# Kernel optimization log

Hardware: AMD Instinct MI355X
Metric: run time of the kernel (lower is better)

Reference implementation:

```python
import jax, jax.numpy as jnp
import numpy as np

B, N, M, C = 8, 2048, 2048, 512


def setup_inputs() -> dict:
    key = jax.random.key(0)
    ks = jax.random.split(key, 10)
    s = 1.0 / np.sqrt(C)
    dec_embed = jax.random.normal(ks[0], (B, N, C), dtype=jnp.float32)
    enc_embed = jax.random.normal(ks[1], (B, M, C), dtype=jnp.float32)
    trans_mat = (jax.random.uniform(ks[2], (B, N, M)) < 0.5).astype(jnp.float32)
    Wv = jax.random.uniform(ks[3], (C, C), minval=-s, maxval=s, dtype=jnp.float32)
    bv = jax.random.uniform(ks[4], (C,), minval=-s, maxval=s, dtype=jnp.float32)
    W1 = jax.random.uniform(ks[5], (C, C), minval=-s, maxval=s, dtype=jnp.float32)
    b1 = jax.random.uniform(ks[6], (C,), minval=-s, maxval=s, dtype=jnp.float32)
    W2 = jax.random.uniform(ks[7], (C, C), minval=-s, maxval=s, dtype=jnp.float32)
    b2 = jax.random.uniform(ks[8], (C,), minval=-s, maxval=s, dtype=jnp.float32)
    return {"dec_embed": dec_embed, "enc_embed": enc_embed, "trans_mat": trans_mat,
            "Wv": Wv, "bv": bv, "W1": W1, "b1": b1, "W2": W2, "b2": b2}


def reference(dec_embed, enc_embed, trans_mat, Wv, bv, W1, b1, W2, b2):
    # scores [B,N,M], elementwise-masked by trans_mat
    attn = jnp.einsum('bnc,bmc->bnm', dec_embed, enc_embed) * trans_mat
    # NONSTANDARD masked softmax: zeros participate in softmax (exp(0)=1 in denom),
    # then positions where attn==0 are re-zeroed.
    sm = jax.nn.softmax(attn, axis=-1)
    attn = jnp.where(attn != 0, sm, jnp.zeros((), attn.dtype))
    v = enc_embed @ Wv + bv                      # [B,M,C]
    v = jnp.tanh(jnp.einsum('bnm,bmc->bnc', attn, v))  # [B,N,C]
    g = dec_embed * v + dec_embed                # tanh-gate + residual
    h = jax.nn.relu(g @ W1 + b1)                 # Mlp fc1 + ReLU (drop=0)
    return h @ W2 + b2                           # Mlp fc2
```

## Files before the change

### kernel.cpp

```cpp
#include <hip/hip_runtime.h>
#include <math.h>

#define Bb 8
#define Nn 2048
#define Mm 2048
#define Cc 512

typedef __attribute__((ext_vector_type(8))) _Float16 hfrag;
typedef __attribute__((ext_vector_type(4))) float f4;
typedef __attribute__((ext_vector_type(4))) _Float16 h4;

__device__ __forceinline__ void gld16(const void* g, void* l) {
    __builtin_amdgcn_global_load_lds(
        (const __attribute__((address_space(1))) void*)g,
        (__attribute__((address_space(3))) void*)l, 16, 0, 0);
}

template<int EPI, int BN, int SWZ>
__global__ __launch_bounds__(256) void gemm_mfma(
    const _Float16* __restrict__ Ah, long sA, int lda,
    const _Float16* __restrict__ Bh, long sB, int ldb,
    const float* __restrict__ aux, long sAux, int ldaux,
    const _Float16* __restrict__ aux2,
    float* __restrict__ mlal,
    void* __restrict__ Cout, long sC, int ldc, int K, int GX)
{
    constexpr int NI = (BN == 128) ? 4 : 2;
    constexpr int NQ = (512 + BN * 4) / 256;

    __shared__ _Float16 As[128 * 32];
    __shared__ _Float16 Bs[BN * 32];

    int bx, by, bz;
    if (SWZ == 1) {
        const int id = blockIdx.x;
        bz = id & 7; bx = (id >> 3) % GX; by = (id >> 3) / GX;
    } else if (SWZ == 2) {
        const int id = blockIdx.x;
        bz = 0; bx = (id >> 3) % GX; by = (id & 7) + 8 * ((id >> 3) / GX);
    } else {
        bx = blockIdx.x; by = blockIdx.y; bz = 0;
    }

    const _Float16* A0 = Ah + (size_t)bz * sA;
    const _Float16* B0 = Bh + (size_t)bz * sB;

    const int tid  = threadIdx.x;
    const int wv   = tid >> 6;
    const int ln   = tid & 63;
    const int wx   = (BN == 128) ? (wv & 1) : 0;
    const int wy   = (BN == 128) ? (wv >> 1) : wv;
    const int lcol = ln & 15, quad = ln >> 4;
    const int row0w = wy * (NI * 16);
    const int col0w = wx * 64;

    const int rowBase = by * 128;
    const int colBase = bx * BN;

    f4 acc[NI][4];
    const f4 z4 = {0.f, 0.f, 0.f, 0.f};
    #pragma unroll
    for (int i = 0; i < NI; ++i)
        #pragma unroll
        for (int j = 0; j < 4; ++j) acc[i][j] = z4;

    const float* alb = (EPI == 2) ? (mlal + (size_t)bz * (2048 * 32)) : nullptr;
    _Float16 als[4] = {(_Float16)0.f, (_Float16)0.f, (_Float16)0.f, (_Float16)0.f};

    for (int k0 = 0; k0 < K; k0 += 32) {
        __syncthreads();
        #pragma unroll
        for (int q = 0; q < NQ; ++q) {
            const int c0 = q * 256 + wv * 64;
            const int c  = c0 + ln;
            if (c0 < 512) {
                const int r  = c >> 2;
                const int ko = (c & 3) * 8;
                gld16(A0 + (size_t)(rowBase + r) * lda + k0 + ko, &As[c0 * 8]);
            } else {
                const int cb = c - 512;
                const int r  = cb >> 2;
                const int ko = (cb & 3) * 8;
                gld16(B0 + (size_t)(colBase + r) * ldb + k0 + ko, &Bs[(c0 - 512) * 8]);
            }
        }
        __syncthreads();

        hfrag af[NI], bf_[4];
        const int aoff = quad * 8;
        #pragma unroll
        for (int i = 0; i < NI; ++i)
            af[i]  = *(const hfrag*)&As[(row0w + i * 16 + lcol) * 32 + aoff];
        #pragma unroll
        for (int j = 0; j < 4; ++j)
            bf_[j] = *(const hfrag*)&Bs[(col0w + j * 16 + lcol) * 32 + aoff];

        if (EPI == 2) {
            if ((k0 & 63) == 0) {
                const int t = k0 >> 6;
                #pragma unroll
                for (int j = 0; j < 4; ++j) {
                    const int n = colBase + col0w + j * 16 + lcol;
                    als[j] = (_Float16)alb[(size_t)n * 32 + t];
                }
            }
            #pragma unroll
            for (int j = 0; j < 4; ++j) bf_[j] = bf_[j] * als[j];
        }

        #pragma unroll
        for (int i = 0; i < NI; ++i)
            #pragma unroll
            for (int j = 0; j < 4; ++j)
                acc[i][j] = __builtin_amdgcn_mfma_f32_16x16x32_f16(af[i], bf_[j], acc[i][j], 0, 0, 0);
    }

    const int crow0 = rowBase + row0w + quad * 4;
    const int ccol0 = colBase + col0w + lcol;

    if (EPI == 0) {
        _Float16* E = (_Float16*)Cout + (size_t)bz * sC;
        const float* Mk = aux + (size_t)bz * sAux;
        #pragma unroll
        for (int i = 0; i < NI; ++i) {
            const int m0r = crow0 + i * 16;
            #pragma unroll
            for (int j = 0; j < 4; ++j) {
                const int n = ccol0 + j * 16;
                const f4 mk = *(const f4*)(Mk + (size_t)n * ldaux + m0r);
                #pragma unroll
                for (int r = 0; r < 4; ++r) acc[i][j][r] *= mk[r];
            }
        }
        const int t = (rowBase + row0w) >> 6;
        #pragma unroll
        for (int j = 0; j < 4; ++j) {
            const int n = ccol0 + j * 16;
            float mx = acc[0][j][0];
            #pragma unroll
            for (int i = 0; i < NI; ++i)
                #pragma unroll
                for (int r = 0; r < 4; ++r) mx = fmaxf(mx, acc[i][j][r]);
            mx = fmaxf(mx, __shfl_xor(mx, 16, 64));
            mx = fmaxf(mx, __shfl_xor(mx, 32, 64));
            float l0 = 0.f;
            #pragma unroll
            for (int i = 0; i < NI; ++i) {
                h4 ev;
                #pragma unroll
                for (int r = 0; r < 4; ++r) {
                    const float s = acc[i][j][r];
                    const float e = __expf(s - mx);
                    l0 += e;
                    ev[r] = (s == 0.f) ? (_Float16)0.f : (_Float16)e;
                }
                *(h4*)(E + (size_t)n * ldc + crow0 + i * 16) = ev;
            }
            l0 += __shfl_xor(l0, 16, 64);
            l0 += __shfl_xor(l0, 32, 64);
            if (quad == 0) {
                float2 p; p.x = mx; p.y = l0;
                ((float2*)mlal)[((size_t)bz * 2048 + n) * 32 + t] = p;
            }
        }
    } else if (EPI == 1) {
        _Float16* C = (_Float16*)Cout;
        #pragma unroll
        for (int j = 0; j < 4; ++j) {
            const int col = ccol0 + j * 16;
            const float bi = aux[col];
            #pragma unroll
            for (int i = 0; i < NI; ++i) {
                const int rowb = crow0 + i * 16;
                const int bb = rowb >> 11, ml = rowb & 2047;
                h4 st;
                #pragma unroll
                for (int r = 0; r < 4; ++r) st[r] = (_Float16)(acc[i][j][r] + bi);
                *(h4*)(C + (size_t)bb * ((size_t)Cc * Mm) + (size_t)col * Mm + ml) = st;
            }
        }
    } else if (EPI == 2) {
        _Float16* C = (_Float16*)Cout + (size_t)bz * sC;
        const _Float16* Dg = aux2 + (size_t)bz * sC;
        #pragma unroll
        for (int i = 0; i < NI; ++i) {
            const int c0 = crow0 + i * 16;
            #pragma unroll
            for (int j = 0; j < 4; ++j) {
                const int n = ccol0 + j * 16;
                const h4 dv = *(const h4*)(Dg + (size_t)n * ldc + c0);
                h4 gv;
                #pragma unroll
                for (int r = 0; r < 4; ++r) {
                    const float a = acc[i][j][r];
                    const float th = 1.f - 2.f / (__expf(2.f * a) + 1.f);
                    gv[r] = (_Float16)((float)dv[r] * (1.f + th));
                }
                *(h4*)(C + (size_t)n * ldc + c0) = gv;
            }
        }
    } else if (EPI == 3) {
        _Float16* C = (_Float16*)Cout;
        #pragma unroll
        for (int i = 0; i < NI; ++i) {
            const int c0 = crow0 + i * 16;
            const f4 bi = *(const f4*)(aux + c0);
            #pragma unroll
            for (int j = 0; j < 4; ++j) {
                const int n = ccol0 + j * 16;
                h4 hv;
                #pragma unroll
                for (int r = 0; r < 4; ++r)
                    hv[r] = (_Float16)fmaxf(acc[i][j][r] + bi[r], 0.f);
                *(h4*)(C + (size_t)n * ldc + c0) = hv;
            }
        }
    } else {
        float* C = (float*)Cout;
        #pragma unroll
        for (int i = 0; i < NI; ++i) {
            const int c0 = crow0 + i * 16;
            const f4 bi = *(const f4*)(aux + c0);
            #pragma unroll
            for (int j = 0; j < 4; ++j) {
                const int n = ccol0 + j * 16;
                f4 ov;
                #pragma unroll
                for (int r = 0; r < 4; ++r) ov[r] = acc[i][j][r] + bi[r];
                *(f4*)(C + (size_t)n * ldc + c0) = ov;
            }
        }
    }
}

__global__ __launch_bounds__(64) void combine_kernel(
    const float* __restrict__ mlq, float* __restrict__ alpha)
{
    const int row = blockIdx.x * 64 + threadIdx.x;
    const float2* ml = (const float2*)mlq + (size_t)row * 32;
    float mt[32], lt[32];
    float m = -1e30f;
    #pragma unroll
    for (int t = 0; t < 32; ++t) {
        float2 p = ml[t];
        mt[t] = p.x; lt[t] = p.y;
        m = fmaxf(m, p.x);
    }
    float et[32], l = 0.f;
    #pragma unroll
    for (int t = 0; t < 32; ++t) {
        et[t] = __expf(mt[t] - m);
        l += lt[t] * et[t];
    }
    const float inv = 1.f / l;
    float* ap = alpha + (size_t)row * 32;
    #pragma unroll
    for (int t = 0; t < 32; ++t) ap[t] = et[t] * inv;
}

__global__ __launch_bounds__(256) void sconv(const float* __restrict__ x,
                                             _Float16* __restrict__ o)
{
    const size_t i = (size_t)blockIdx.x * 256 + threadIdx.x;
    f4 v = ((const f4*)x)[i];
    h4 hh;
    #pragma unroll
    for (int k = 0; k < 4; ++k) hh[k] = (_Float16)v[k];
    ((h4*)o)[i] = hh;
}

__global__ __launch_bounds__(256) void wconv(const float* s0, const float* s1, const float* s2,
                                             _Float16* d0, _Float16* d1, _Float16* d2)
{
    const float* Sm = blockIdx.z == 0 ? s0 : blockIdx.z == 1 ? s1 : s2;
    _Float16* D = blockIdx.z == 0 ? d0 : blockIdx.z == 1 ? d1 : d2;
    __shared__ float t[32][33];
    const int x = threadIdx.x & 31, y = threadIdx.x >> 5;
    const int gx = blockIdx.x * 32, gy = blockIdx.y * 32;
    #pragma unroll
    for (int yy = y; yy < 32; yy += 8)
        t[yy][x] = Sm[(size_t)(gy + yy) * 512 + gx + x];
    __syncthreads();
    #pragma unroll
    for (int yy = y; yy < 32; yy += 8)
        D[(size_t)(gx + yy) * 512 + gy + x] = (_Float16)t[x][yy];
}

extern "C" void kernel_launch(void* const* d_in, const int* in_sizes, int n_in,
                              void* d_out, int out_size, void* d_ws, size_t ws_size,
                              hipStream_t stream)
{
    const float* dec   = (const float*)d_in[0];
    const float* enc   = (const float*)d_in[1];
    const float* trans = (const float*)d_in[2];
    const float* Wv = (const float*)d_in[3];
    const float* bv = (const float*)d_in[4];
    const float* W1 = (const float*)d_in[5];
    const float* b1 = (const float*)d_in[6];
    const float* W2 = (const float*)d_in[7];
    const float* b2 = (const float*)d_in[8];

    char* ws = (char*)d_ws;
    _Float16* e     = (_Float16*)ws;
    float*    mlq   = (float*)(ws + 0x4000000);
    float*    alpha = (float*)(ws + 0x4400000);
    _Float16* dec_h = (_Float16*)(ws + 0x4600000);
    _Float16* Wvt   = (_Float16*)(ws + 0x5600000);
    _Float16* W1t   = Wvt + 262144;
    _Float16* W2t   = Wvt + 524288;
    _Float16* vT    = (_Float16*)(ws + 0x5800000);
    _Float16* g     = (_Float16*)(ws + 0x6800000);
    _Float16* h     = (_Float16*)(ws + 0x7800000);
    _Float16* enc_h = (_Float16*)d_out;

    sconv<<<dim3(8192), 256, 0, stream>>>(dec, dec_h);
    sconv<<<dim3(8192), 256, 0, stream>>>(enc, enc_h);
    wconv<<<dim3(16, 16, 3), 256, 0, stream>>>(Wv, W1, W2, Wvt, W1t, W2t);

    gemm_mfma<0, 128, 1><<<dim3(2048), 256, 0, stream>>>(
        enc_h, (long)Mm * Cc, 512,
        dec_h, (long)Nn * Cc, 512,
        trans, (long)Nn * Mm, 2048, nullptr, mlq,
        e, (long)Nn * Mm, 2048, 512, 16);

    combine_kernel<<<dim3(256), 64, 0, stream>>>(mlq, alpha);

    gemm_mfma<1, 64, 2><<<dim3(1024), 256, 0, stream>>>(
        enc_h, 0, 512, Wvt, 0, 512, bv, 0, 0, nullptr, nullptr,
        vT, 0, 0, 512, 8);

    gemm_mfma<2, 128, 1><<<dim3(512), 256, 0, stream>>>(
        vT, (long)Cc * Mm, 2048,
        e, (long)Nn * Mm, 2048,
        nullptr, 0, 512, dec_h, alpha,
        g, (long)Nn * Cc, 512, 2048, 16);

    gemm_mfma<3, 64, 0><<<dim3(256, 4), 256, 0, stream>>>(
        W1t, 0, 512, g, 0, 512, b1, 0, 0, nullptr, nullptr,
        h, 0, 512, 512, 0);

    gemm_mfma<4, 64, 0><<<dim3(256, 4), 256, 0, stream>>>(
        W2t, 0, 512, h, 0, 512, b2, 0, 0, nullptr, nullptr,
        d_out, 0, 512, 512, 0);
}
```

Baseline: 460.3 us.

## Double K-tile depth per sync and software-pipeline mask loads in softmax epilogue

The GEMM main loop now stages a 64-wide K slice (two 32-wide halves) into doubled LDS buffers per iteration, which halves the number of barrier pairs and global-to-LDS issue rounds. The EPI==2 alpha scale load is hoisted to once per 64-K step. In the EPI==0 epilogue, mask loads are restructured so the loads for the next column group are issued before the current group's max/exp work, letting their latency overlap. The cost is more LDS per block and more registers live in the epilogue, which may reduce occupancy.

After: 436.4 us. 5.2% less time.

```diff
diff --git a/kernel.cpp b/kernel.cpp
--- a/kernel.cpp
+++ b/kernel.cpp
@@ -26,10 +26,10 @@
     void* __restrict__ Cout, long sC, int ldc, int K, int GX)
 {
     constexpr int NI = (BN == 128) ? 4 : 2;
-    constexpr int NQ = (512 + BN * 4) / 256;
-
-    __shared__ _Float16 As[128 * 32];
-    __shared__ _Float16 Bs[BN * 32];
+    constexpr int NQ = (1024 + BN * 8) / 256;
+
+    __shared__ _Float16 As[2 * 128 * 32];
+    __shared__ _Float16 Bs[2 * BN * 32];
 
     int bx, by, bz;
     if (SWZ == 1) {
@@ -67,52 +67,58 @@
     const float* alb = (EPI == 2) ? (mlal + (size_t)bz * (2048 * 32)) : nullptr;
     _Float16 als[4] = {(_Float16)0.f, (_Float16)0.f, (_Float16)0.f, (_Float16)0.f};
 
-    for (int k0 = 0; k0 < K; k0 += 32) {
+    for (int k0 = 0; k0 < K; k0 += 64) {
         __syncthreads();
         #pragma unroll
         for (int q = 0; q < NQ; ++q) {
             const int c0 = q * 256 + wv * 64;
             const int c  = c0 + ln;
-            if (c0 < 512) {
-                const int r  = c >> 2;
-                const int ko = (c & 3) * 8;
+            if (c0 < 1024) {
+                const int hh = c >> 9;
+                const int r  = (c >> 2) & 127;
+                const int ko = hh * 32 + (c & 3) * 8;
                 gld16(A0 + (size_t)(rowBase + r) * lda + k0 + ko, &As[c0 * 8]);
             } else {
-                const int cb = c - 512;
-                const int r  = cb >> 2;
-                const int ko = (cb & 3) * 8;
-                gld16(B0 + (size_t)(colBase + r) * ldb + k0 + ko, &Bs[(c0 - 512) * 8]);
+                const int cb = c - 1024;
+                const int hh = cb / (BN * 4);
+                const int r  = (cb >> 2) & (BN - 1);
+                const int ko = hh * 32 + (cb & 3) * 8;
+                gld16(B0 + (size_t)(colBase + r) * ldb + k0 + ko, &Bs[(c0 - 1024) * 8]);
             }
         }
         __syncthreads();
 
-        hfrag af[NI], bf_[4];
-        const int aoff = quad * 8;
-        #pragma unroll
-        for (int i = 0; i < NI; ++i)
-            af[i]  = *(const hfrag*)&As[(row0w + i * 16 + lcol) * 32 + aoff];
-        #pragma unroll
-        for (int j = 0; j < 4; ++j)
-            bf_[j] = *(const hfrag*)&Bs[(col0w + j * 16 + lcol) * 32 + aoff];
-
         if (EPI == 2) {
-            if ((k0 & 63) == 0) {
-                const int t = k0 >> 6;
-                #pragma unroll
-                for (int j = 0; j < 4; ++j) {
-                    const int n = colBase + col0w + j * 16 + lcol;
-                    als[j] = (_Float16)alb[(size_t)n * 32 + t];
-                }
-            }
-            #pragma unroll
-            for (int j = 0; j < 4; ++j) bf_[j] = bf_[j] * als[j];
-        }
-
-        #pragma unroll
-        for (int i = 0; i < NI; ++i)
+            const int t = k0 >> 6;
+            #pragma unroll
+            for (int j = 0; j < 4; ++j) {
+                const int n = colBase + col0w + j * 16 + lcol;
+                als[j] = (_Float16)alb[(size_t)n * 32 + t];
+            }
+        }
+
+        #pragma unroll
+        for (int hh = 0; hh < 2; ++hh) {
+            hfrag af[NI], bf_[4];
+            const int aoff = quad * 8;
+            #pragma unroll
+            for (int i = 0; i < NI; ++i)
+                af[i]  = *(const hfrag*)&As[hh * 4096 + (row0w + i * 16 + lcol) * 32 + aoff];
             #pragma unroll
             for (int j = 0; j < 4; ++j)
-                acc[i][j] = __builtin_amdgcn_mfma_f32_16x16x32_f16(af[i], bf_[j], acc[i][j], 0, 0, 0);
+                bf_[j] = *(const hfrag*)&Bs[hh * (BN * 32) + (col0w + j * 16 + lcol) * 32 + aoff];
+
+            if (EPI == 2) {
+                #pragma unroll
+                for (int j = 0; j < 4; ++j) bf_[j] = bf_[j] * als[j];
+            }
+
+            #pragma unroll
+            for (int i = 0; i < NI; ++i)
+                #pragma unroll
+                for (int j = 0; j < 4; ++j)
+                    acc[i][j] = __builtin_amdgcn_mfma_f32_16x16x32_f16(af[i], bf_[j], acc[i][j], 0, 0, 0);
+        }
     }
 
     const int crow0 = rowBase + row0w + quad * 4;
@@ -121,21 +127,27 @@
     if (EPI == 0) {
         _Float16* E = (_Float16*)Cout + (size_t)bz * sC;
         const float* Mk = aux + (size_t)bz * sAux;
-        #pragma unroll
-        for (int i = 0; i < NI; ++i) {
-            const int m0r = crow0 + i * 16;
-            #pragma unroll
-            for (int j = 0; j < 4; ++j) {
-                const int n = ccol0 + j * 16;
-                const f4 mk = *(const f4*)(Mk + (size_t)n * ldaux + m0r);
-                #pragma unroll
-                for (int r = 0; r < 4; ++r) acc[i][j][r] *= mk[r];
-            }
-        }
         const int t = (rowBase + row0w) >> 6;
+
+        f4 mk[NI];
+        #pragma unroll
+        for (int i = 0; i < NI; ++i)
+            mk[i] = *(const f4*)(Mk + (size_t)ccol0 * ldaux + crow0 + i * 16);
+
         #pragma unroll
         for (int j = 0; j < 4; ++j) {
             const int n = ccol0 + j * 16;
+            f4 mkn[NI];
+            if (j < 3) {
+                #pragma unroll
+                for (int i = 0; i < NI; ++i)
+                    mkn[i] = *(const f4*)(Mk + (size_t)(n + 16) * ldaux + crow0 + i * 16);
+            }
+            #pragma unroll
+            for (int i = 0; i < NI; ++i)
+                #pragma unroll
+                for (int r = 0; r < 4; ++r) acc[i][j][r] *= mk[i][r];
+
             float mx = acc[0][j][0];
             #pragma unroll
             for (int i = 0; i < NI; ++i)
@@ -161,6 +173,10 @@
             if (quad == 0) {
                 float2 p; p.x = mx; p.y = l0;
                 ((float2*)mlal)[((size_t)bz * 2048 + n) * 32 + t] = p;
+            }
+            if (j < 3) {
+                #pragma unroll
+                for (int i = 0; i < NI; ++i) mk[i] = mkn[i];
             }
         }
     } else if (EPI == 1) {
```
